# Kernel optimization log

Measured on AMD Instinct MI355X. Metric: run time of the kernel, lower is better.

The kernel has to match this reference:

```python
import jax, jax.numpy as jnp
import numpy as np

B, S, E, H = 2, 2048, 1024, 16
D = E // H  # head_dim = 64


def setup_inputs() -> dict:
    key = jax.random.key(0)
    ks = jax.random.split(key, 6)
    sc = 0.02
    return {
        "hidden_states": jax.random.normal(ks[0], (B, S, E), dtype=jnp.float32),
        "attn_bias": jax.random.normal(ks[1], (S, S), dtype=jnp.float32) * sc,
        "Wqkv": jax.random.normal(ks[2], (E, 3 * E), dtype=jnp.float32) * sc,
        "bqkv": jax.random.normal(ks[3], (3 * E,), dtype=jnp.float32) * sc,
        "Wproj": jax.random.normal(ks[4], (E, E), dtype=jnp.float32) * sc,
        "bproj": jax.random.normal(ks[5], (E,), dtype=jnp.float32) * sc,
    }


def reference(hidden_states, attn_bias, Wqkv, bqkv, Wproj, bproj):
    b, s, e = hidden_states.shape
    qkv = hidden_states @ Wqkv + bqkv                      # [b,s,3e]
    q, k, v = jnp.split(qkv, 3, axis=-1)                   # each [b,s,e]
    cache_key, cache_value = k, v                          # kvCache
    # [b,h,s,d]
    qh = q.reshape(b, s, H, D).transpose(0, 2, 1, 3)
    kh = k.reshape(b, s, H, D).transpose(0, 2, 1, 3)
    vh = v.reshape(b, s, H, D).transpose(0, 2, 1, 3)
    scores = jnp.einsum("bhqd,bhkd->bhqk", qh, kh) / jnp.sqrt(jnp.float32(D))
    scores = scores + attn_bias[:s, :s][None, None]        # learned additive bias
    causal = jnp.tril(jnp.ones((s, s), dtype=bool))
    scores = jnp.where(causal[None, None], scores, jnp.float32(-1e9))
    attn = jax.nn.softmax(scores, axis=-1)
    ctx = jnp.einsum("bhqk,bhkd->bhqd", attn, vh)
    ctx = ctx.transpose(0, 2, 1, 3).reshape(b, s, e)
    out = ctx @ Wproj + bproj                              # resid dropout p=0 -> identity
    return (out, cache_key, cache_value)
```

## Files before the change

kernel.cpp:

```cpp
#include <hip/hip_runtime.h>

#define B_ 2
#define S_ 2048
#define E_ 1024
#define H_ 16
#define D_ 64

typedef short  s16x8 __attribute__((ext_vector_type(8)));
typedef float  f32x4 __attribute__((ext_vector_type(4)));
typedef unsigned short u16x4 __attribute__((ext_vector_type(4)));

__device__ __forceinline__ ushort f2bf(float f) {
    union { float f; unsigned u; } x; x.f = f;
    unsigned u = x.u + 0x7fffu + ((x.u >> 16) & 1u);
    return (ushort)(u >> 16);
}

__device__ __forceinline__ float fast_exp2(float x) {
    float r; asm("v_exp_f32 %0, %1" : "=v"(r) : "v"(x)); return r;
}

__global__ __launch_bounds__(256) void prep_fused_kernel(
    const float* __restrict__ X, ushort* __restrict__ Xbf,
    const float* __restrict__ Wqkv, ushort* __restrict__ Wqkvt,
    const float* __restrict__ Wproj, ushort* __restrict__ Wprojt)
{
    __shared__ float tile[64][65];
    int blk = blockIdx.x;
    int tid = threadIdx.x;
    if (blk < 4096) {
        int i = (blk * 256 + tid) * 4;
        float4 v = *(const float4*)&X[i];
        u16x4 o;
        o.x = f2bf(v.x); o.y = f2bf(v.y); o.z = f2bf(v.z); o.w = f2bf(v.w);
        *(u16x4*)&Xbf[i] = o;
        return;
    }
    const float* W; ushort* Wt; int Ndim, nb;
    if (blk < 4096 + 768) { blk -= 4096; W = Wqkv;  Wt = Wqkvt;  Ndim = 3 * E_; nb = 48; }
    else                  { blk -= 4864; W = Wproj; Wt = Wprojt; Ndim = E_;     nb = 16; }
    int n0 = (blk % nb) * 64, k0 = (blk / nb) * 64;
    int c = tid & 63;
#pragma unroll
    for (int r = tid >> 6; r < 64; r += 4)
        tile[r][c] = W[(size_t)(k0 + r) * Ndim + n0 + c];
    __syncthreads();
#pragma unroll
    for (int r = tid >> 6; r < 64; r += 4)
        Wt[(size_t)(n0 + r) * E_ + k0 + c] = f2bf(tile[c][r]);
}

__global__ __launch_bounds__(256) void post_qkv_kernel(
    const float* __restrict__ V, ushort* __restrict__ Vt,
    const float* __restrict__ bias, ushort* __restrict__ biasT)
{
    __shared__ float tile[64][65];
    int blk = blockIdx.x;
    int tid = threadIdx.x;
    if (blk < 1024) {
        int s0 = (blk & 31) * 64;
        int bh = blk >> 5;
        int b = bh >> 4, h = bh & 15;
        int d = tid & 63;
#pragma unroll
        for (int i = tid >> 6; i < 64; i += 4)
            tile[i][d] = V[((size_t)(b * S_ + s0 + i)) * E_ + h * 64 + d];
        __syncthreads();
        int lane = tid & 63, w = tid >> 6;
        int g = lane >> 5, rem = lane & 31, q2 = rem >> 3, i2 = rem & 7;
        int src = (2 * g + (i2 >> 2)) * 16 + q2 * 4 + (i2 & 3);
#pragma unroll
        for (int dd = w; dd < 64; dd += 4)
            Vt[((size_t)(bh * 64 + dd)) * S_ + s0 + lane] = f2bf(tile[src][dd]);
        return;
    }
    int L = blk - 1024;
    int qi = (int)((sqrtf(8.0f * (float)L + 1.0f) - 1.0f) * 0.5f);
    while ((qi + 1) * (qi + 2) / 2 <= L) qi++;
    while (qi * (qi + 1) / 2 > L) qi--;
    int ki = L - qi * (qi + 1) / 2;
    int w = tid >> 6, quad = (tid >> 4) & 3, l15 = tid & 15;
    const float LOG2E = 1.4426950408889634f;
    s16x8 h0 = (s16x8){0,0,0,0,0,0,0,0}, h1 = (s16x8){0,0,0,0,0,0,0,0};
#pragma unroll
    for (int kt = 0; kt < 4; kt++) {
        float4 v4 = *(const float4*)&bias[(size_t)(qi * 64 + w * 16 + l15) * S_
                                          + ki * 64 + kt * 16 + quad * 4];
        ushort u0 = f2bf(v4.x * LOG2E);
        ushort u1 = f2bf(v4.y * LOG2E);
        ushort u2 = f2bf(v4.z * LOG2E);
        ushort u3 = f2bf(v4.w * LOG2E);
        if (kt < 2) {
            h0[kt * 4 + 0] = (short)u0; h0[kt * 4 + 1] = (short)u1;
            h0[kt * 4 + 2] = (short)u2; h0[kt * 4 + 3] = (short)u3;
        } else {
            h1[(kt - 2) * 4 + 0] = (short)u0; h1[(kt - 2) * 4 + 1] = (short)u1;
            h1[(kt - 2) * 4 + 2] = (short)u2; h1[(kt - 2) * 4 + 3] = (short)u3;
        }
    }
    ushort* dst = &biasT[((size_t)L * 256 + tid) * 16];
    *(s16x8*)dst = h0;
    *(s16x8*)(dst + 8) = h1;
}

__global__ __launch_bounds__(256) void gemm_mfma_bt(
    const ushort* __restrict__ A,
    const ushort* __restrict__ Bt,
    const float* __restrict__ bias,
    int M, int N, int K,
    float* __restrict__ C0,
    ushort* __restrict__ Qbf, float* __restrict__ Kf32, ushort* __restrict__ Kbf,
    float* __restrict__ Vf32, int mode)
{
    __shared__ ushort As[128 * 64];
    __shared__ ushort Bs[128 * 64];
    int tid = threadIdx.x;
    int wid = tid >> 6, lane = tid & 63;
    int l15 = lane & 15, quad = lane >> 4;
    int wm = wid >> 1, wn = wid & 1;
    int row0 = blockIdx.y * 128, col0 = blockIdx.x * 128;

    int srow = tid >> 3;
    int pk = (tid & 7) * 8;
    int sk = (((tid & 7) ^ (srow & 7)) * 8);

    f32x4 acc[4][4];
#pragma unroll
    for (int mt = 0; mt < 4; mt++)
#pragma unroll
        for (int nt = 0; nt < 4; nt++) acc[mt][nt] = (f32x4){0.f, 0.f, 0.f, 0.f};

    for (int k0 = 0; k0 < K; k0 += 64) {
        __syncthreads();
#pragma unroll
        for (int c = 0; c < 4; c++) {
            int r = c * 32 + srow;
            __builtin_amdgcn_global_load_lds(
                (const __attribute__((address_space(1))) unsigned int*)
                    &A[(size_t)(row0 + r) * K + k0 + sk],
                (__attribute__((address_space(3))) unsigned int*)&As[r * 64 + pk],
                16, 0, 0);
            __builtin_amdgcn_global_load_lds(
                (const __attribute__((address_space(1))) unsigned int*)
                    &Bt[(size_t)(col0 + r) * K + k0 + sk],
                (__attribute__((address_space(3))) unsigned int*)&Bs[r * 64 + pk],
                16, 0, 0);
        }
        __syncthreads();

#pragma unroll
        for (int kk = 0; kk < 2; kk++) {
            int xc = (((kk * 4 + quad) ^ (l15 & 7)) * 8);
            s16x8 af[4], bf[4];
#pragma unroll
            for (int mt = 0; mt < 4; mt++)
                af[mt] = *(const s16x8*)&As[(wm * 64 + mt * 16 + l15) * 64 + xc];
#pragma unroll
            for (int nt = 0; nt < 4; nt++)
                bf[nt] = *(const s16x8*)&Bs[(wn * 64 + nt * 16 + l15) * 64 + xc];
#pragma unroll
            for (int mt = 0; mt < 4; mt++)
#pragma unroll
                for (int nt = 0; nt < 4; nt++)
                    acc[mt][nt] = __builtin_amdgcn_mfma_f32_16x16x32_bf16(
                        af[mt], bf[nt], acc[mt][nt], 0, 0, 0);
        }
    }

#pragma unroll
    for (int nt = 0; nt < 4; nt++) {
        int n = col0 + wn * 64 + nt * 16 + l15;
        float bv = bias[n];
        if (mode == 1) {
            int seg = n >> 10;
            int nn = n & (E_ - 1);
#pragma unroll
            for (int mt = 0; mt < 4; mt++)
#pragma unroll
                for (int r = 0; r < 4; r++) {
                    int row = row0 + wm * 64 + mt * 16 + quad * 4 + r;
                    float v = acc[mt][nt][r] + bv;
                    size_t idx = (size_t)row * E_ + nn;
                    if (seg == 0)      Qbf[idx] = f2bf(v);
                    else if (seg == 1) { Kf32[idx] = v; Kbf[idx] = f2bf(v); }
                    else               Vf32[idx] = v;
                }
        } else {
#pragma unroll
            for (int mt = 0; mt < 4; mt++)
#pragma unroll
                for (int r = 0; r < 4; r++) {
                    int row = row0 + wm * 64 + mt * 16 + quad * 4 + r;
                    C0[(size_t)row * N + n] = acc[mt][nt][r] + bv;
                }
        }
    }
}

__global__ __launch_bounds__(256) void attn_mfma_kernel(
    const ushort* __restrict__ Qbf,
    const ushort* __restrict__ Kbf,
    const ushort* __restrict__ Vt,
    const ushort* __restrict__ biasT,
    ushort* __restrict__ Ctx)
{
    __shared__ ushort Ks[64][64];
    __shared__ ushort Vs[64][64];

    int blk = blockIdx.x;
    int bh = blk & 31;
    int pr = blk >> 5;
    int b = bh >> 4, h = bh & 15;
    int tid = threadIdx.x;
    int wid = tid >> 6, lane = tid & 63;
    int l15 = lane & 15, quad = lane >> 4;

    int skey = tid >> 2;
    int scol = (tid & 3) * 16;
    int sc0 = ((((tid & 3) * 2) ^ (skey & 7)) * 8);
    int sc1 = sc0 ^ 8;
    const float scale_l2e = 0.18033688011112042f;

    const size_t krow = (size_t)(b * S_ + skey) * E_ + h * 64 + scol;
    const size_t vrow = (size_t)(bh * 64 + skey) * S_ + scol;
    int rc0 = (quad ^ (l15 & 7)) * 8;

    for (int half = 0; half < 2; half++) {
        int qt = half ? pr : (31 - pr);
        int q0w = qt * 64 + wid * 16;
        int rowq = q0w + l15;

        const size_t qbase = ((size_t)(b * S_ + q0w + l15)) * E_ + h * 64 + quad * 8;
        s16x8 qa0 = *(const s16x8*)&Qbf[qbase];
        s16x8 qa1 = *(const s16x8*)&Qbf[qbase + 32];

        f32x4 o[4];
#pragma unroll
        for (int dt = 0; dt < 4; dt++) o[dt] = (f32x4){0.f, 0.f, 0.f, 0.f};
        float ls = 0.f;

        float4 kr0 = ((const float4*)&Kbf[krow])[0];
        float4 kr1 = ((const float4*)&Kbf[krow])[1];
        float4 vr0 = ((const float4*)&Vt[vrow])[0];
        float4 vr1 = ((const float4*)&Vt[vrow])[1];
        const ushort* bt = &biasT[((size_t)(qt * (qt + 1) / 2) * 256 + tid) * 16];
        s16x8 bn0 = *(const s16x8*)bt;
        s16x8 bn1 = *(const s16x8*)(bt + 8);

        for (int t = 0; t <= qt; t++) {
            int j0 = t * 64;
            __syncthreads();
            *(float4*)&Ks[skey][sc0] = kr0;
            *(float4*)&Ks[skey][sc1] = kr1;
            *(float4*)&Vs[skey][sc0] = vr0;
            *(float4*)&Vs[skey][sc1] = vr1;
            s16x8 b0 = bn0, b1 = bn1;
            __syncthreads();

            if (t < qt) {
                int j1 = j0 + 64;
                kr0 = ((const float4*)&Kbf[krow + (size_t)j1 * E_])[0];
                kr1 = ((const float4*)&Kbf[krow + (size_t)j1 * E_])[1];
                vr0 = ((const float4*)&Vt[vrow + j1])[0];
                vr1 = ((const float4*)&Vt[vrow + j1])[1];
                const ushort* btn = bt + (size_t)(t + 1) * 4096;
                bn0 = *(const s16x8*)btn;
                bn1 = *(const s16x8*)(btn + 8);
            }

            f32x4 s[4];
#pragma unroll
            for (int kt = 0; kt < 4; kt++) {
                s16x8 kb0 = *(const s16x8*)&Ks[kt * 16 + l15][rc0];
                s16x8 kb1 = *(const s16x8*)&Ks[kt * 16 + l15][rc0 ^ 32];
                f32x4 acc = (f32x4){0.f, 0.f, 0.f, 0.f};
                acc = __builtin_amdgcn_mfma_f32_16x16x32_bf16(kb0, qa0, acc, 0, 0, 0);
                acc = __builtin_amdgcn_mfma_f32_16x16x32_bf16(kb1, qa1, acc, 0, 0, 0);
                s[kt] = acc;
            }

            bool diag = (t == qt);
            unsigned upk[8];
#pragma unroll
            for (int kt = 0; kt < 4; kt++) {
                float pv[4];
#pragma unroll
                for (int r = 0; r < 4; r++) {
                    int idx = kt * 4 + r;
                    ushort ub = (ushort)((idx < 8) ? b0[idx] : b1[idx - 8]);
                    union { unsigned u; float f; } bc; bc.u = ((unsigned)ub) << 16;
                    float v = fmaf(s[kt][r], scale_l2e, bc.f);
                    int j = j0 + kt * 16 + quad * 4 + r;
                    float p = (diag && j > rowq) ? 0.f : fast_exp2(v);
                    ls += p;
                    pv[r] = p;
                }
                asm("v_cvt_pk_bf16_f32 %0, %1, %2"
                    : "=v"(upk[kt * 2]) : "v"(pv[0]), "v"(pv[1]));
                asm("v_cvt_pk_bf16_f32 %0, %1, %2"
                    : "=v"(upk[kt * 2 + 1]) : "v"(pv[2]), "v"(pv[3]));
            }
            uint4 ua = make_uint4(upk[0], upk[1], upk[2], upk[3]);
            uint4 ub4 = make_uint4(upk[4], upk[5], upk[6], upk[7]);
            s16x8 pa0 = *(s16x8*)&ua;
            s16x8 pa1 = *(s16x8*)&ub4;

#pragma unroll
            for (int dt = 0; dt < 4; dt++) {
                s16x8 vb0 = *(const s16x8*)&Vs[dt * 16 + l15][rc0];
                s16x8 vb1 = *(const s16x8*)&Vs[dt * 16 + l15][rc0 ^ 32];
                o[dt] = __builtin_amdgcn_mfma_f32_16x16x32_bf16(pa0, vb0, o[dt], 0, 0, 0);
                o[dt] = __builtin_amdgcn_mfma_f32_16x16x32_bf16(pa1, vb1, o[dt], 0, 0, 0);
            }
        }

        float l = ls;
        l += __shfl_xor(l, 16);
        l += __shfl_xor(l, 32);
        float inv = 1.f / l;
        float inv_l[4];
#pragma unroll
        for (int r = 0; r < 4; r++)
            inv_l[r] = __shfl(inv, quad * 4 + r);

#pragma unroll
        for (int dt = 0; dt < 4; dt++) {
#pragma unroll
            for (int r = 0; r < 4; r++) {
                int row = q0w + quad * 4 + r;
                Ctx[((size_t)(b * S_ + row)) * E_ + h * 64 + dt * 16 + l15] =
                    f2bf(o[dt][r] * inv_l[r]);
            }
        }
    }
}

extern "C" void kernel_launch(void* const* d_in, const int* in_sizes, int n_in,
                              void* d_out, int out_size, void* d_ws, size_t ws_size,
                              hipStream_t stream) {
    const float* X     = (const float*)d_in[0];
    const float* abias = (const float*)d_in[1];
    const float* Wqkv  = (const float*)d_in[2];
    const float* bqkv  = (const float*)d_in[3];
    const float* Wproj = (const float*)d_in[4];
    const float* bproj = (const float*)d_in[5];

    const size_t plane = (size_t)B_ * S_ * E_;
    float* out  = (float*)d_out;
    float* kout = out + plane;
    float* vout = kout + plane;

    ushort* xbf    = (ushort*)d_ws;
    ushort* qbf    = xbf + plane;
    ushort* kbf    = qbf + plane;
    ushort* vt     = kbf + plane;
    ushort* ctxbf  = xbf;
    ushort* wqkvt  = vt + plane;
    ushort* wprojt = wqkvt + (size_t)3 * E_ * E_;
    ushort* biasT  = wqkvt;

    const int M = B_ * S_;

    prep_fused_kernel<<<dim3(5120), 256, 0, stream>>>(
        X, xbf, Wqkv, wqkvt, Wproj, wprojt);

    gemm_mfma_bt<<<dim3(3 * E_ / 128, M / 128), 256, 0, stream>>>(
        xbf, wqkvt, bqkv, M, 3 * E_, E_,
        nullptr, qbf, kout, kbf, vout, 1);

    post_qkv_kernel<<<dim3(1024 + 528), 256, 0, stream>>>(
        vout, vt, abias, biasT);

    attn_mfma_kernel<<<dim3(B_ * H_ * 16), 256, 0, stream>>>(
        qbf, kbf, vt, biasT, ctxbf);

    gemm_mfma_bt<<<dim3(E_ / 128, M / 128), 256, 0, stream>>>(
        ctxbf, wprojt, bproj, M, E_, E_,
        out, nullptr, nullptr, nullptr, nullptr, 0);
}
```

Measured before the change: 214.6 us.

## Fuse V transpose into QKV GEMM epilogue and use 64-row tiles for projection

```diff
diff --git a/kernel.cpp b/kernel.cpp
--- a/kernel.cpp
+++ b/kernel.cpp
@@ -50,35 +50,15 @@
         Wt[(size_t)(n0 + r) * E_ + k0 + c] = f2bf(tile[c][r]);
 }
 
-__global__ __launch_bounds__(256) void post_qkv_kernel(
-    const float* __restrict__ V, ushort* __restrict__ Vt,
+__global__ __launch_bounds__(256) void prep_bias_kernel(
     const float* __restrict__ bias, ushort* __restrict__ biasT)
 {
-    __shared__ float tile[64][65];
-    int blk = blockIdx.x;
-    int tid = threadIdx.x;
-    if (blk < 1024) {
-        int s0 = (blk & 31) * 64;
-        int bh = blk >> 5;
-        int b = bh >> 4, h = bh & 15;
-        int d = tid & 63;
-#pragma unroll
-        for (int i = tid >> 6; i < 64; i += 4)
-            tile[i][d] = V[((size_t)(b * S_ + s0 + i)) * E_ + h * 64 + d];
-        __syncthreads();
-        int lane = tid & 63, w = tid >> 6;
-        int g = lane >> 5, rem = lane & 31, q2 = rem >> 3, i2 = rem & 7;
-        int src = (2 * g + (i2 >> 2)) * 16 + q2 * 4 + (i2 & 3);
-#pragma unroll
-        for (int dd = w; dd < 64; dd += 4)
-            Vt[((size_t)(bh * 64 + dd)) * S_ + s0 + lane] = f2bf(tile[src][dd]);
-        return;
-    }
-    int L = blk - 1024;
+    int L = blockIdx.x;
     int qi = (int)((sqrtf(8.0f * (float)L + 1.0f) - 1.0f) * 0.5f);
     while ((qi + 1) * (qi + 2) / 2 <= L) qi++;
     while (qi * (qi + 1) / 2 > L) qi--;
     int ki = L - qi * (qi + 1) / 2;
+    int tid = threadIdx.x;
     int w = tid >> 6, quad = (tid >> 4) & 3, l15 = tid & 15;
     const float LOG2E = 1.4426950408889634f;
     s16x8 h0 = (s16x8){0,0,0,0,0,0,0,0}, h1 = (s16x8){0,0,0,0,0,0,0,0};
@@ -108,9 +88,8 @@
     const ushort* __restrict__ Bt,
     const float* __restrict__ bias,
     int M, int N, int K,
-    float* __restrict__ C0,
     ushort* __restrict__ Qbf, float* __restrict__ Kf32, ushort* __restrict__ Kbf,
-    float* __restrict__ Vf32, int mode)
+    float* __restrict__ Vf32, ushort* __restrict__ Vt)
 {
     __shared__ ushort As[128 * 64];
     __shared__ ushort Bs[128 * 64];
@@ -171,29 +150,116 @@
     for (int nt = 0; nt < 4; nt++) {
         int n = col0 + wn * 64 + nt * 16 + l15;
         float bv = bias[n];
-        if (mode == 1) {
-            int seg = n >> 10;
-            int nn = n & (E_ - 1);
-#pragma unroll
-            for (int mt = 0; mt < 4; mt++)
-#pragma unroll
-                for (int r = 0; r < 4; r++) {
-                    int row = row0 + wm * 64 + mt * 16 + quad * 4 + r;
-                    float v = acc[mt][nt][r] + bv;
-                    size_t idx = (size_t)row * E_ + nn;
-                    if (seg == 0)      Qbf[idx] = f2bf(v);
-                    else if (seg == 1) { Kf32[idx] = v; Kbf[idx] = f2bf(v); }
-                    else               Vf32[idx] = v;
-                }
-        } else {
-#pragma unroll
-            for (int mt = 0; mt < 4; mt++)
-#pragma unroll
-                for (int r = 0; r < 4; r++) {
-                    int row = row0 + wm * 64 + mt * 16 + quad * 4 + r;
-                    C0[(size_t)row * N + n] = acc[mt][nt][r] + bv;
-                }
-        }
+        int seg = n >> 10;
+        int nn = n & (E_ - 1);
+#pragma unroll
+        for (int mt = 0; mt < 4; mt++) {
+            float v4[4];
+#pragma unroll
+            for (int r = 0; r < 4; r++) {
+                int row = row0 + wm * 64 + mt * 16 + quad * 4 + r;
+                float v = acc[mt][nt][r] + bv;
+                v4[r] = v;
+                size_t idx = (size_t)row * E_ + nn;
+                if (seg == 0)      Qbf[idx] = f2bf(v);
+                else if (seg == 1) { Kf32[idx] = v; Kbf[idx] = f2bf(v); }
+                else               Vf32[idx] = v;
+            }
+            if (seg == 2) {
+                int row_base = row0 + wm * 64;
+                int b = row_base >> 11;
+                int h = nn >> 6, d = nn & 63;
+                int stile = (row_base & 2047) >> 6;
+                int slot = ((mt >> 1) * 32) + quad * 8 + ((mt & 1) * 4);
+                unsigned w0, w1;
+                asm("v_cvt_pk_bf16_f32 %0, %1, %2" : "=v"(w0) : "v"(v4[0]), "v"(v4[1]));
+                asm("v_cvt_pk_bf16_f32 %0, %1, %2" : "=v"(w1) : "v"(v4[2]), "v"(v4[3]));
+                uint2 wv; wv.x = w0; wv.y = w1;
+                size_t vtidx = ((size_t)((b * 16 + h) * 64 + d)) * S_
+                               + stile * 64 + slot;
+                *(uint2*)&Vt[vtidx] = wv;
+            }
+        }
+    }
+}
+
+__global__ __launch_bounds__(256) void gemm_proj64(
+    const ushort* __restrict__ A,
+    const ushort* __restrict__ Bt,
+    const float* __restrict__ bias,
+    int M, int N, int K,
+    float* __restrict__ C0)
+{
+    __shared__ ushort As[64 * 64];
+    __shared__ ushort Bs[128 * 64];
+    int tid = threadIdx.x;
+    int wid = tid >> 6, lane = tid & 63;
+    int l15 = lane & 15, quad = lane >> 4;
+    int wm = wid >> 1, wn = wid & 1;
+    int row0 = blockIdx.y * 64, col0 = blockIdx.x * 128;
+
+    int srow = tid >> 3;
+    int pk = (tid & 7) * 8;
+    int sk = (((tid & 7) ^ (srow & 7)) * 8);
+
+    f32x4 acc[2][4];
+#pragma unroll
+    for (int mt = 0; mt < 2; mt++)
+#pragma unroll
+        for (int nt = 0; nt < 4; nt++) acc[mt][nt] = (f32x4){0.f, 0.f, 0.f, 0.f};
+
+    for (int k0 = 0; k0 < K; k0 += 64) {
+        __syncthreads();
+#pragma unroll
+        for (int c = 0; c < 2; c++) {
+            int r = c * 32 + srow;
+            __builtin_amdgcn_global_load_lds(
+                (const __attribute__((address_space(1))) unsigned int*)
+                    &A[(size_t)(row0 + r) * K + k0 + sk],
+                (__attribute__((address_space(3))) unsigned int*)&As[r * 64 + pk],
+                16, 0, 0);
+        }
+#pragma unroll
+        for (int c = 0; c < 4; c++) {
+            int r = c * 32 + srow;
+            __builtin_amdgcn_global_load_lds(
+                (const __attribute__((address_space(1))) unsigned int*)
+                    &Bt[(size_t)(col0 + r) * K + k0 + sk],
+                (__attribute__((address_space(3))) unsigned int*)&Bs[r * 64 + pk],
+                16, 0, 0);
+        }
+        __syncthreads();
+
+#pragma unroll
+        for (int kk = 0; kk < 2; kk++) {
+            int xc = (((kk * 4 + quad) ^ (l15 & 7)) * 8);
+            s16x8 af[2], bf[4];
+#pragma unroll
+            for (int mt = 0; mt < 2; mt++)
+                af[mt] = *(const s16x8*)&As[(wm * 32 + mt * 16 + l15) * 64 + xc];
+#pragma unroll
+            for (int nt = 0; nt < 4; nt++)
+                bf[nt] = *(const s16x8*)&Bs[(wn * 64 + nt * 16 + l15) * 64 + xc];
+#pragma unroll
+            for (int mt = 0; mt < 2; mt++)
+#pragma unroll
+                for (int nt = 0; nt < 4; nt++)
+                    acc[mt][nt] = __builtin_amdgcn_mfma_f32_16x16x32_bf16(
+                        af[mt], bf[nt], acc[mt][nt], 0, 0, 0);
+        }
+    }
+
+#pragma unroll
+    for (int nt = 0; nt < 4; nt++) {
+        int n = col0 + wn * 64 + nt * 16 + l15;
+        float bv = bias[n];
+#pragma unroll
+        for (int mt = 0; mt < 2; mt++)
+#pragma unroll
+            for (int r = 0; r < 4; r++) {
+                int row = row0 + wm * 32 + mt * 16 + quad * 4 + r;
+                C0[(size_t)row * N + n] = acc[mt][nt][r] + bv;
+            }
     }
 }
 
@@ -366,15 +432,13 @@
 
     gemm_mfma_bt<<<dim3(3 * E_ / 128, M / 128), 256, 0, stream>>>(
         xbf, wqkvt, bqkv, M, 3 * E_, E_,
-        nullptr, qbf, kout, kbf, vout, 1);
-
-    post_qkv_kernel<<<dim3(1024 + 528), 256, 0, stream>>>(
-        vout, vt, abias, biasT);
+        qbf, kout, kbf, vout, vt);
+
+    prep_bias_kernel<<<dim3(528), 256, 0, stream>>>(abias, biasT);
 
     attn_mfma_kernel<<<dim3(B_ * H_ * 16), 256, 0, stream>>>(
         qbf, kbf, vt, biasT, ctxbf);
 
-    gemm_mfma_bt<<<dim3(E_ / 128, M / 128), 256, 0, stream>>>(
-        ctxbf, wprojt, bproj, M, E_, E_,
-        out, nullptr, nullptr, nullptr, nullptr, 0);
-}
+    gemm_proj64<<<dim3(E_ / 128, M / 64), 256, 0, stream>>>(
+        ctxbf, wprojt, bproj, M, E_, E_, out);
+}
```

Measured after the change: 210.4 us. 1.02x faster.
